# Kernel tuning notes

Hardware: AMD Instinct MI355X
Metric: run time of the kernel (lower is better)

The kernel has to match this reference:

```python
import jax, jax.numpy as jnp
import numpy as np

# Matcher hyperparameters (from __init__ defaults)
COST_CLASS = 1.0
COST_CENTER = 5.0
COST_IOU = 2.0
CENTER_THRESHOLD = 2.0
INF_REPLACE = 1000000.0

B, Q, N, NUM_CLASSES = 64, 4096, 256, 20
SCENE_EXTENT = 50.0  # meters; box centers uniform in [0, 50]


def setup_inputs() -> dict:
    key = jax.random.key(0)
    k1, k2, k3, k4, k5, k6 = jax.random.split(key, 6)
    pred_logits = jax.random.normal(k1, (B, Q, NUM_CLASSES + 1), dtype=jnp.float32)
    pred_centers = jax.random.uniform(k2, (B, Q, 3), dtype=jnp.float32) * SCENE_EXTENT
    pred_sizes = jax.random.uniform(k3, (B, Q, 3), dtype=jnp.float32) * 2.5 + 0.5
    pred_boxes = jnp.concatenate([pred_centers, pred_sizes], axis=-1)  # [B,Q,6]
    tgt_centers = jax.random.uniform(k4, (B, N, 3), dtype=jnp.float32) * SCENE_EXTENT
    tgt_sizes = jax.random.uniform(k5, (B, N, 3), dtype=jnp.float32) * 2.5 + 0.5
    target_boxes = jnp.concatenate([tgt_centers, tgt_sizes], axis=-1)  # [B,N,6]
    target_labels = jax.random.randint(k6, (B, N), 0, NUM_CLASSES)  # all valid fg classes
    return {
        "pred_logits": pred_logits,
        "pred_boxes": pred_boxes,
        "target_labels": target_labels,
        "target_boxes": target_boxes,
    }


def _pairwise_iou3d(pred_boxes, target_boxes):
    # pred_boxes [B,Q,6], target_boxes [B,N,6] -> iou [B,Q,N]
    c1, s1 = pred_boxes[..., :3], pred_boxes[..., 3:]
    c2, s2 = target_boxes[..., :3], target_boxes[..., 3:]
    min1 = (c1 - s1 * 0.5)[:, :, None, :]  # [B,Q,1,3]
    max1 = (c1 + s1 * 0.5)[:, :, None, :]
    min2 = (c2 - s2 * 0.5)[:, None, :, :]  # [B,1,N,3]
    max2 = (c2 + s2 * 0.5)[:, None, :, :]
    inter_size = jnp.clip(jnp.minimum(max1, max2) - jnp.maximum(min1, min2), 0.0)
    inter_vol = jnp.prod(inter_size, axis=-1)  # [B,Q,N]
    vol1 = jnp.prod(s1, axis=-1)[:, :, None]  # [B,Q,1]
    vol2 = jnp.prod(s2, axis=-1)[:, None, :]  # [B,1,N]
    union = vol1 + vol2 - inter_vol
    return jnp.where(union > 0, inter_vol / union, 0.0)


def reference(pred_logits, pred_boxes, target_labels, target_boxes):
    # Class cost: -softmax prob of the target's class (foreground classes only)
    probs_fg = jax.nn.softmax(pred_logits, axis=-1)[..., :-1]  # [B,Q,C]
    class_cost = -jax.vmap(lambda p, l: p[:, l])(probs_fg, target_labels)  # [B,Q,N]

    # Center distance cost with threshold gating (torch.cdist = euclidean)
    pc = pred_boxes[..., :3]
    tc = target_boxes[..., :3]
    dist = jnp.sqrt(jnp.sum((pc[:, :, None, :] - tc[:, None, :, :]) ** 2, axis=-1))
    center_cost = jnp.where(dist <= CENTER_THRESHOLD, dist, jnp.inf)

    # 3D IoU cost
    iou_cost = 1.0 - _pairwise_iou3d(pred_boxes, target_boxes)

    total = COST_CLASS * class_cost + COST_CENTER * center_cost + COST_IOU * iou_cost
    total = jnp.where(jnp.isinf(total), INF_REPLACE, total)
    return total  # [B,Q,N] cost matrix fed to the (CPU) Hungarian solver
```

## Files before the change

kernel.cpp:

```cpp
#include <hip/hip_runtime.h>
#include <math.h>

#define BQ 64
#define QQ 4096
#define NN 256
#define NC 20
#define NL 21
#define TQ 256
#define GEO_STRIDE 12
#define PROB_STRIDE 257

#define GATE_D2 0x1.000001p+2f

__global__ __launch_bounds__(256)
void matcher_kernel(const float* __restrict__ logits,
                    const float* __restrict__ pboxes,
                    const int*   __restrict__ tlabels,
                    const float* __restrict__ tboxes,
                    float* __restrict__ out) {
    __shared__ __align__(16) float geo[TQ * GEO_STRIDE];
    __shared__ float prob[NC * PROB_STRIDE];
    const int tid = threadIdx.x;
    const int b   = blockIdx.y;
    const int q0  = blockIdx.x * TQ;

    {
        const int q = q0 + tid;
        const float* lg = logits + (size_t)(b * QQ + q) * NL;
        float l[NL];
        #pragma unroll
        for (int c = 0; c < NL; ++c) l[c] = lg[c];
        float m = l[0];
        #pragma unroll
        for (int c = 1; c < NL; ++c) m = fmaxf(m, l[c]);
        float e[NL];
        float s = 0.f;
        #pragma unroll
        for (int c = 0; c < NL; ++c) { e[c] = expf(l[c] - m); s += e[c]; }
        const float rs = 1.0f / s;
        #pragma unroll
        for (int c = 0; c < NC; ++c)
            prob[c * PROB_STRIDE + tid] = -(e[c] * rs);

        const float* pb = pboxes + (size_t)(b * QQ + q) * 6;
        const float pcx = pb[0], pcy = pb[1], pcz = pb[2];
        const float psx = pb[3], psy = pb[4], psz = pb[5];
        float4* gp = (float4*)(geo + tid * GEO_STRIDE);
        gp[0] = make_float4(pcx, pcy, pcz, psx * psy * psz);
        gp[1] = make_float4(pcx - psx * 0.5f, pcy - psy * 0.5f, pcz - psz * 0.5f, 0.f);
        gp[2] = make_float4(pcx + psx * 0.5f, pcy + psy * 0.5f, pcz + psz * 0.5f, 0.f);
    }

    const int lane = tid & 63;
    const int w    = tid >> 6;
    const int n0   = lane * 4;
    float tcx[4], tcy[4], tcz[4];
    float mn_x[4], mn_y[4], mn_z[4], mx_x[4], mx_y[4], mx_z[4], v2[4];
    int plab[4];
    #pragma unroll
    for (int j = 0; j < 4; ++j) {
        const float* tb = tboxes + (size_t)(b * NN + n0 + j) * 6;
        const float cx = tb[0], cy = tb[1], cz = tb[2];
        const float sx = tb[3], sy = tb[4], sz = tb[5];
        tcx[j] = cx; tcy[j] = cy; tcz[j] = cz;
        mn_x[j] = cx - sx * 0.5f; mn_y[j] = cy - sy * 0.5f; mn_z[j] = cz - sz * 0.5f;
        mx_x[j] = cx + sx * 0.5f; mx_y[j] = cy + sy * 0.5f; mx_z[j] = cz + sz * 0.5f;
        v2[j]   = sx * sy * sz;
        plab[j] = tlabels[b * NN + n0 + j] * PROB_STRIDE;
    }

    __syncthreads();

    const float4 MISS = make_float4(1000000.0f, 1000000.0f, 1000000.0f, 1000000.0f);
    float* ob = out + ((size_t)(b * QQ + q0)) * NN + n0;

    for (int qq = w; qq < TQ; qq += 4) {
        const float4* gp = (const float4*)(geo + qq * GEO_STRIDE);
        const float4 g0 = gp[0];

        float d2v[4];
        int active = 0;
        #pragma unroll
        for (int j = 0; j < 4; ++j) {
            const float dx = __fsub_rn(g0.x, tcx[j]);
            const float dy = __fsub_rn(g0.y, tcy[j]);
            const float dz = __fsub_rn(g0.z, tcz[j]);
            d2v[j] = __fadd_rn(__fadd_rn(__fmul_rn(dx, dx), __fmul_rn(dy, dy)),
                               __fmul_rn(dz, dz));
            active |= (d2v[j] <= GATE_D2);
        }

        float4* orow = (float4*)(ob + (size_t)qq * NN);
        if (!__any(active)) {
            *orow = MISS;
            continue;
        }

        const float4 g1 = gp[1];
        const float4 g2 = gp[2];
        float r[4];
        #pragma unroll
        for (int j = 0; j < 4; ++j) {
            const float negp = prob[plab[j] + qq];

            const float dist = __builtin_amdgcn_sqrtf(d2v[j]);

            const float ix = fmaxf(fminf(g2.x, mx_x[j]) - fmaxf(g1.x, mn_x[j]), 0.f);
            const float iy = fmaxf(fminf(g2.y, mx_y[j]) - fmaxf(g1.y, mn_y[j]), 0.f);
            const float iz = fmaxf(fminf(g2.z, mx_z[j]) - fmaxf(g1.z, mn_z[j]), 0.f);
            const float iv  = ix * iy * iz;
            const float uni = g0.w + v2[j] - iv;
            const float iou = iv * __builtin_amdgcn_rcpf(uni);

            const float t = fmaf(5.0f, dist, negp) + fmaf(-2.0f, iou, 2.0f);
            r[j] = (d2v[j] <= GATE_D2) ? t : 1000000.0f;
        }
        *orow = make_float4(r[0], r[1], r[2], r[3]);
    }
}

extern "C" void kernel_launch(void* const* d_in, const int* in_sizes, int n_in,
                              void* d_out, int out_size, void* d_ws, size_t ws_size,
                              hipStream_t stream) {
    const float* logits  = (const float*)d_in[0];
    const float* pboxes  = (const float*)d_in[1];
    const int*   tlabels = (const int*)d_in[2];
    const float* tboxes  = (const float*)d_in[3];
    float* out = (float*)d_out;

    dim3 grid(QQ / TQ, BQ);
    matcher_kernel<<<grid, dim3(256), 0, stream>>>(logits, pboxes, tlabels, tboxes, out);
}
```

Before: 295.1 us.

## Compute softmax lazily only for query rows with gated-in targets

Drops the per-block softmax prologue and its shared-memory probability table. Each wave now loads the query's logits and computes the softmax only when some target passes the center-distance gate for that row. The target's class probability is picked with a register select chain instead of an LDS lookup. The change also vectorises box loads to float2 and adds an occupancy hint to launch bounds. The savings are logits traffic and exp work for rows that end up all-miss, plus lower LDS use. In exchange, active rows do redundant per-lane softmax and a longer select chain.

```diff
diff --git a/kernel.cpp b/kernel.cpp
--- a/kernel.cpp
+++ b/kernel.cpp
@@ -8,43 +8,26 @@
 #define NL 21
 #define TQ 256
 #define GEO_STRIDE 12
-#define PROB_STRIDE 257
 
 #define GATE_D2 0x1.000001p+2f
 
-__global__ __launch_bounds__(256)
+__global__ __launch_bounds__(256, 6)
 void matcher_kernel(const float* __restrict__ logits,
                     const float* __restrict__ pboxes,
                     const int*   __restrict__ tlabels,
                     const float* __restrict__ tboxes,
                     float* __restrict__ out) {
     __shared__ __align__(16) float geo[TQ * GEO_STRIDE];
-    __shared__ float prob[NC * PROB_STRIDE];
     const int tid = threadIdx.x;
     const int b   = blockIdx.y;
     const int q0  = blockIdx.x * TQ;
 
     {
         const int q = q0 + tid;
-        const float* lg = logits + (size_t)(b * QQ + q) * NL;
-        float l[NL];
-        #pragma unroll
-        for (int c = 0; c < NL; ++c) l[c] = lg[c];
-        float m = l[0];
-        #pragma unroll
-        for (int c = 1; c < NL; ++c) m = fmaxf(m, l[c]);
-        float e[NL];
-        float s = 0.f;
-        #pragma unroll
-        for (int c = 0; c < NL; ++c) { e[c] = expf(l[c] - m); s += e[c]; }
-        const float rs = 1.0f / s;
-        #pragma unroll
-        for (int c = 0; c < NC; ++c)
-            prob[c * PROB_STRIDE + tid] = -(e[c] * rs);
-
-        const float* pb = pboxes + (size_t)(b * QQ + q) * 6;
-        const float pcx = pb[0], pcy = pb[1], pcz = pb[2];
-        const float psx = pb[3], psy = pb[4], psz = pb[5];
+        const float2* pb = (const float2*)(pboxes + (size_t)(b * QQ + q) * 6);
+        const float2 p01 = pb[0], p23 = pb[1], p45 = pb[2];
+        const float pcx = p01.x, pcy = p01.y, pcz = p23.x;
+        const float psx = p23.y, psy = p45.x, psz = p45.y;
         float4* gp = (float4*)(geo + tid * GEO_STRIDE);
         gp[0] = make_float4(pcx, pcy, pcz, psx * psy * psz);
         gp[1] = make_float4(pcx - psx * 0.5f, pcy - psy * 0.5f, pcz - psz * 0.5f, 0.f);
@@ -56,17 +39,18 @@
     const int n0   = lane * 4;
     float tcx[4], tcy[4], tcz[4];
     float mn_x[4], mn_y[4], mn_z[4], mx_x[4], mx_y[4], mx_z[4], v2[4];
-    int plab[4];
+    int lab[4];
     #pragma unroll
     for (int j = 0; j < 4; ++j) {
-        const float* tb = tboxes + (size_t)(b * NN + n0 + j) * 6;
-        const float cx = tb[0], cy = tb[1], cz = tb[2];
-        const float sx = tb[3], sy = tb[4], sz = tb[5];
+        const float2* tb = (const float2*)(tboxes + (size_t)(b * NN + n0 + j) * 6);
+        const float2 t01 = tb[0], t23 = tb[1], t45 = tb[2];
+        const float cx = t01.x, cy = t01.y, cz = t23.x;
+        const float sx = t23.y, sy = t45.x, sz = t45.y;
         tcx[j] = cx; tcy[j] = cy; tcz[j] = cz;
         mn_x[j] = cx - sx * 0.5f; mn_y[j] = cy - sy * 0.5f; mn_z[j] = cz - sz * 0.5f;
         mx_x[j] = cx + sx * 0.5f; mx_y[j] = cy + sy * 0.5f; mx_z[j] = cz + sz * 0.5f;
         v2[j]   = sx * sy * sz;
-        plab[j] = tlabels[b * NN + n0 + j] * PROB_STRIDE;
+        lab[j]  = tlabels[b * NN + n0 + j];
     }
 
     __syncthreads();
@@ -74,6 +58,7 @@
     const float4 MISS = make_float4(1000000.0f, 1000000.0f, 1000000.0f, 1000000.0f);
     float* ob = out + ((size_t)(b * QQ + q0)) * NN + n0;
 
+    #pragma unroll 1
     for (int qq = w; qq < TQ; qq += 4) {
         const float4* gp = (const float4*)(geo + qq * GEO_STRIDE);
         const float4 g0 = gp[0];
@@ -96,12 +81,27 @@
             continue;
         }
 
+        const float* lg = logits + (size_t)(b * QQ + q0 + qq) * NL;
+        float e[NL];
+        #pragma unroll
+        for (int c = 0; c < NL; ++c) e[c] = lg[c];
+        float m = e[0];
+        #pragma unroll
+        for (int c = 1; c < NL; ++c) m = fmaxf(m, e[c]);
+        float s = 0.f;
+        #pragma unroll
+        for (int c = 0; c < NL; ++c) { e[c] = expf(e[c] - m); s += e[c]; }
+        const float rs = 1.0f / s;
+
         const float4 g1 = gp[1];
         const float4 g2 = gp[2];
         float r[4];
         #pragma unroll
         for (int j = 0; j < 4; ++j) {
-            const float negp = prob[plab[j] + qq];
+            float ev = e[0];
+            #pragma unroll
+            for (int c = 1; c < NC; ++c) ev = (lab[j] == c) ? e[c] : ev;
+            const float negp = -(ev * rs);
 
             const float dist = __builtin_amdgcn_sqrtf(d2v[j]);
 
```

New measurement: 314.8 us. 1.07x slower.

## Add per-batch voxel occupancy mask to skip unreachable query rows

Applied to the files above, without the earlier changes.

Adds a pre-pass kernel that builds a 50^3-cell bitmask per batch marking cells within the gating radius of any target center. The matcher then looks up each query's cell and writes the miss row directly when the cell is empty, skipping the distance and IoU evaluation for that row. The aim is to cut ALU work for queries far from every target. It adds an extra launch and a workspace dependency, and it assumes box centers lie within [0,50], which the clamping only partly guards. The kernel is still bound by writing the full output matrix, so the saving may be small.

```diff
diff --git a/kernel.cpp b/kernel.cpp
--- a/kernel.cpp
+++ b/kernel.cpp
@@ -12,14 +12,60 @@
 
 #define GATE_D2 0x1.000001p+2f
 
+#define MCELLS 50
+#define MWORDS 3907
+#define MSTRIDE 3920
+#define MMARGIN 4.05f
+
+__global__ __launch_bounds__(256)
+void mask_kernel(const float* __restrict__ tboxes, unsigned* __restrict__ gmask) {
+    __shared__ unsigned sm[MWORDS];
+    const int tid = threadIdx.x;
+    const int b   = blockIdx.x;
+    for (int i = tid; i < MWORDS; i += 256) sm[i] = 0u;
+    __syncthreads();
+
+    const float* tb = tboxes + (size_t)(b * NN + tid) * 6;
+    const float tx = tb[0], ty = tb[1], tz = tb[2];
+    int x0 = (int)floorf(tx - 2.f); x0 = x0 < 0 ? 0 : x0;
+    int x1 = (int)floorf(tx + 2.f); x1 = x1 > MCELLS - 1 ? MCELLS - 1 : x1;
+    int y0 = (int)floorf(ty - 2.f); y0 = y0 < 0 ? 0 : y0;
+    int y1 = (int)floorf(ty + 2.f); y1 = y1 > MCELLS - 1 ? MCELLS - 1 : y1;
+    int z0 = (int)floorf(tz - 2.f); z0 = z0 < 0 ? 0 : z0;
+    int z1 = (int)floorf(tz + 2.f); z1 = z1 > MCELLS - 1 ? MCELLS - 1 : z1;
+
+    #pragma unroll 1
+    for (int i = x0; i <= x1; ++i) {
+        const float dx = fmaxf(fmaxf((float)i - tx, tx - (float)(i + 1)), 0.f);
+        #pragma unroll 1
+        for (int j = y0; j <= y1; ++j) {
+            const float dy = fmaxf(fmaxf((float)j - ty, ty - (float)(j + 1)), 0.f);
+            #pragma unroll 1
+            for (int k = z0; k <= z1; ++k) {
+                const float dz = fmaxf(fmaxf((float)k - tz, tz - (float)(k + 1)), 0.f);
+                const float d2 = dx * dx + dy * dy + dz * dz;
+                if (d2 <= MMARGIN) {
+                    const int idx = (i * MCELLS + j) * MCELLS + k;
+                    atomicOr(&sm[idx >> 5], 1u << (idx & 31));
+                }
+            }
+        }
+    }
+    __syncthreads();
+    unsigned* gb = gmask + (size_t)b * MSTRIDE;
+    for (int i = tid; i < MWORDS; i += 256) gb[i] = sm[i];
+}
+
 __global__ __launch_bounds__(256)
 void matcher_kernel(const float* __restrict__ logits,
                     const float* __restrict__ pboxes,
                     const int*   __restrict__ tlabels,
                     const float* __restrict__ tboxes,
+                    const unsigned* __restrict__ gmask,
                     float* __restrict__ out) {
     __shared__ __align__(16) float geo[TQ * GEO_STRIDE];
     __shared__ float prob[NC * PROB_STRIDE];
+    __shared__ int actq[TQ];
     const int tid = threadIdx.x;
     const int b   = blockIdx.y;
     const int q0  = blockIdx.x * TQ;
@@ -49,6 +95,16 @@
         gp[0] = make_float4(pcx, pcy, pcz, psx * psy * psz);
         gp[1] = make_float4(pcx - psx * 0.5f, pcy - psy * 0.5f, pcz - psz * 0.5f, 0.f);
         gp[2] = make_float4(pcx + psx * 0.5f, pcy + psy * 0.5f, pcz + psz * 0.5f, 0.f);
+
+        int flag = 1;
+        if (gmask) {
+            int cx = (int)pcx; cx = cx > MCELLS - 1 ? MCELLS - 1 : cx;
+            int cy = (int)pcy; cy = cy > MCELLS - 1 ? MCELLS - 1 : cy;
+            int cz = (int)pcz; cz = cz > MCELLS - 1 ? MCELLS - 1 : cz;
+            const int idx = (cx * MCELLS + cy) * MCELLS + cz;
+            flag = (int)((gmask[(size_t)b * MSTRIDE + (idx >> 5)] >> (idx & 31)) & 1u);
+        }
+        actq[tid] = flag;
     }
 
     const int lane = tid & 63;
@@ -74,7 +130,15 @@
     const float4 MISS = make_float4(1000000.0f, 1000000.0f, 1000000.0f, 1000000.0f);
     float* ob = out + ((size_t)(b * QQ + q0)) * NN + n0;
 
+    #pragma unroll 1
     for (int qq = w; qq < TQ; qq += 4) {
+        float4* orow = (float4*)(ob + (size_t)qq * NN);
+
+        if (actq[qq] == 0) {
+            *orow = MISS;
+            continue;
+        }
+
         const float4* gp = (const float4*)(geo + qq * GEO_STRIDE);
         const float4 g0 = gp[0];
 
@@ -90,7 +154,6 @@
             active |= (d2v[j] <= GATE_D2);
         }
 
-        float4* orow = (float4*)(ob + (size_t)qq * NN);
         if (!__any(active)) {
             *orow = MISS;
             continue;
@@ -128,6 +191,13 @@
     const float* tboxes  = (const float*)d_in[3];
     float* out = (float*)d_out;
 
+    unsigned* gmask = nullptr;
+    if (ws_size >= (size_t)BQ * MSTRIDE * sizeof(unsigned)) {
+        gmask = (unsigned*)d_ws;
+        mask_kernel<<<dim3(BQ), dim3(256), 0, stream>>>(tboxes, gmask);
+    }
+
     dim3 grid(QQ / TQ, BQ);
-    matcher_kernel<<<grid, dim3(256), 0, stream>>>(logits, pboxes, tlabels, tboxes, out);
+    matcher_kernel<<<grid, dim3(256), 0, stream>>>(logits, pboxes, tlabels, tboxes,
+                                                   gmask, out);
 }
```

Result: slower. 310.9 us (+5.4%).

## Shrink query tile, reload target boxes lazily, and transpose prob layout

Applied to the files above, without the earlier changes.

Reduces the query tile from 256 to 64 per block, so only the first wavefront computes softmax while the block keeps 256 threads, and each wave handles a contiguous run of 16 queries. Target box extents and labels are no longer kept in registers; they are reloaded from global memory inside the rare active branch. The probability array is stored query-major. The aim is fewer registers and less shared memory per block for higher occupancy and a 4x larger grid. The cost is repeated global loads on active rows, and softmax work now runs on only a quarter of each block's threads.

```diff
diff --git a/kernel.cpp b/kernel.cpp
--- a/kernel.cpp
+++ b/kernel.cpp
@@ -6,25 +6,25 @@
 #define NN 256
 #define NC 20
 #define NL 21
-#define TQ 256
+#define TQ 64
 #define GEO_STRIDE 12
-#define PROB_STRIDE 257
+#define PSTR 20
 
 #define GATE_D2 0x1.000001p+2f
 
-__global__ __launch_bounds__(256)
+__global__ __launch_bounds__(256, 8)
 void matcher_kernel(const float* __restrict__ logits,
                     const float* __restrict__ pboxes,
                     const int*   __restrict__ tlabels,
                     const float* __restrict__ tboxes,
                     float* __restrict__ out) {
     __shared__ __align__(16) float geo[TQ * GEO_STRIDE];
-    __shared__ float prob[NC * PROB_STRIDE];
+    __shared__ float prob[TQ * PSTR];
     const int tid = threadIdx.x;
     const int b   = blockIdx.y;
     const int q0  = blockIdx.x * TQ;
 
-    {
+    if (tid < TQ) {
         const int q = q0 + tid;
         const float* lg = logits + (size_t)(b * QQ + q) * NL;
         float l[NL];
@@ -40,7 +40,7 @@
         const float rs = 1.0f / s;
         #pragma unroll
         for (int c = 0; c < NC; ++c)
-            prob[c * PROB_STRIDE + tid] = -(e[c] * rs);
+            prob[tid * PSTR + c] = -(e[c] * rs);
 
         const float* pb = pboxes + (size_t)(b * QQ + q) * 6;
         const float pcx = pb[0], pcy = pb[1], pcz = pb[2];
@@ -55,18 +55,10 @@
     const int w    = tid >> 6;
     const int n0   = lane * 4;
     float tcx[4], tcy[4], tcz[4];
-    float mn_x[4], mn_y[4], mn_z[4], mx_x[4], mx_y[4], mx_z[4], v2[4];
-    int plab[4];
     #pragma unroll
     for (int j = 0; j < 4; ++j) {
         const float* tb = tboxes + (size_t)(b * NN + n0 + j) * 6;
-        const float cx = tb[0], cy = tb[1], cz = tb[2];
-        const float sx = tb[3], sy = tb[4], sz = tb[5];
-        tcx[j] = cx; tcy[j] = cy; tcz[j] = cz;
-        mn_x[j] = cx - sx * 0.5f; mn_y[j] = cy - sy * 0.5f; mn_z[j] = cz - sz * 0.5f;
-        mx_x[j] = cx + sx * 0.5f; mx_y[j] = cy + sy * 0.5f; mx_z[j] = cz + sz * 0.5f;
-        v2[j]   = sx * sy * sz;
-        plab[j] = tlabels[b * NN + n0 + j] * PROB_STRIDE;
+        tcx[j] = tb[0]; tcy[j] = tb[1]; tcz[j] = tb[2];
     }
 
     __syncthreads();
@@ -74,7 +66,9 @@
     const float4 MISS = make_float4(1000000.0f, 1000000.0f, 1000000.0f, 1000000.0f);
     float* ob = out + ((size_t)(b * QQ + q0)) * NN + n0;
 
-    for (int qq = w; qq < TQ; qq += 4) {
+    const int rend = w * 16 + 16;
+    #pragma unroll 1
+    for (int qq = w * 16; qq < rend; ++qq) {
         const float4* gp = (const float4*)(geo + qq * GEO_STRIDE);
         const float4 g0 = gp[0];
 
@@ -101,15 +95,22 @@
         float r[4];
         #pragma unroll
         for (int j = 0; j < 4; ++j) {
-            const float negp = prob[plab[j] + qq];
+            const float* tb = tboxes + (size_t)(b * NN + n0 + j) * 6;
+            const float cx = tb[0], cy = tb[1], cz = tb[2];
+            const float sx = tb[3], sy = tb[4], sz = tb[5];
+            const float mnx = cx - sx * 0.5f, mny = cy - sy * 0.5f, mnz = cz - sz * 0.5f;
+            const float mxx = cx + sx * 0.5f, mxy = cy + sy * 0.5f, mxz = cz + sz * 0.5f;
+            const float v2  = sx * sy * sz;
+            const int  lab  = tlabels[b * NN + n0 + j];
+            const float negp = prob[qq * PSTR + lab];
 
             const float dist = __builtin_amdgcn_sqrtf(d2v[j]);
 
-            const float ix = fmaxf(fminf(g2.x, mx_x[j]) - fmaxf(g1.x, mn_x[j]), 0.f);
-            const float iy = fmaxf(fminf(g2.y, mx_y[j]) - fmaxf(g1.y, mn_y[j]), 0.f);
-            const float iz = fmaxf(fminf(g2.z, mx_z[j]) - fmaxf(g1.z, mn_z[j]), 0.f);
+            const float ix = fmaxf(fminf(g2.x, mxx) - fmaxf(g1.x, mnx), 0.f);
+            const float iy = fmaxf(fminf(g2.y, mxy) - fmaxf(g1.y, mny), 0.f);
+            const float iz = fmaxf(fminf(g2.z, mxz) - fmaxf(g1.z, mnz), 0.f);
             const float iv  = ix * iy * iz;
-            const float uni = g0.w + v2[j] - iv;
+            const float uni = g0.w + v2 - iv;
             const float iou = iv * __builtin_amdgcn_rcpf(uni);
 
             const float t = fmaf(5.0f, dist, negp) + fmaf(-2.0f, iou, 2.0f);
```

After: 299.6 us. Within noise of the previous version (+1.5%).
